# Kernel optimization log

Hardware: AMD Instinct MI355X
Metric: run time of the kernel (lower is better)

The kernel has to match this reference:

```python
import jax, jax.numpy as jnp
import numpy as np
import math

PHI = (1.0 + math.sqrt(5.0)) / 2.0
BASE_FAST = PHI
BASE_SLOW = 1618.0
D = 1024
NH = 16
HD = D // NH
H_GATE = max(8, D // 4)
B, L = 2, 2048


def _rope_cos_sin(seq_len, dim, base):
    # dim assumed even here (D=1024)
    idx = jnp.arange(0, dim, 2, dtype=jnp.float32) / float(dim)
    inv = 1.0 / (base ** idx)
    t = jnp.arange(seq_len, dtype=jnp.float32)
    freqs = jnp.outer(t, inv)                      # (L, dim/2)
    emb = jnp.concatenate([freqs, freqs], axis=-1) # (L, dim)
    return jnp.cos(emb), jnp.sin(emb)


def _rotate_half(x):
    d = x.shape[-1]
    x1, x2 = x[..., : d // 2], x[..., d // 2 :]
    return jnp.concatenate([-x2, x1], axis=-1)


def setup_inputs() -> dict:
    key = jax.random.key(0)
    ks = jax.random.split(key, 16)
    std = 0.02
    inp = {
        "z": jax.random.normal(ks[0], (B, L, D), jnp.float32),
        "pool_seq": jax.random.normal(ks[1], (B, L, D), jnp.float32),
        "Wq": std * jax.random.normal(ks[2], (D, D), jnp.float32),
        "bq": jnp.zeros((D,), jnp.float32),
        "Wk": std * jax.random.normal(ks[3], (D, D), jnp.float32),
        "bk": jnp.zeros((D,), jnp.float32),
        "Wv": std * jax.random.normal(ks[4], (D, D), jnp.float32),
        "bv": jnp.zeros((D,), jnp.float32),
        "W_coh": std * jax.random.normal(ks[5], (D, D), jnp.float32),
        "gamma": jnp.zeros((1,), jnp.float32) + 0.1,  # nonzero so bias path is exercised
        "Wg1": std * jax.random.normal(ks[6], (H_GATE, D), jnp.float32),
        "bg1": jnp.zeros((H_GATE,), jnp.float32),
        "Wg2": std * jax.random.normal(ks[7], (1, H_GATE), jnp.float32),
        "bg2": jnp.zeros((1,), jnp.float32),
    }
    return inp


def reference(z, pool_seq, Wq, bq, Wk, bk, Wv, bv, W_coh, gamma, Wg1, bg1, Wg2, bg2):
    b, l, d = z.shape
    # QKV projections (torch Linear: x @ W^T + b)
    Q = z @ Wq.T + bq
    K_raw = z @ Wk.T + bk
    V = z @ Wv.T + bv

    # Global coherence bias: per-query pool vector dotted with every key
    gk = pool_seq @ W_coh.T                                   # (B,L,D)
    gb = jnp.einsum("bqd,bkd->bqk", gk, K_raw) * (d ** -0.5)  # (B,L,L)
    gb = jnp.tanh(gamma[0]) * gb

    # Per-position RoPE interpolation gate (exact GELU as in torch default)
    h = jax.nn.gelu(pool_seq @ Wg1.T + bg1, approximate=False)
    gate = jax.nn.sigmoid(h @ Wg2.T + bg2)                    # (B,L,1)

    cos_f, sin_f = _rope_cos_sin(l, d, BASE_FAST)             # (L,D)
    cos_s, sin_s = _rope_cos_sin(l, d, BASE_SLOW)
    cos = gate * cos_f + (1.0 - gate) * cos_s                 # (B,L,D)
    sin = gate * sin_f + (1.0 - gate) * sin_s

    Q = Q * cos + _rotate_half(Q) * sin
    K_rot = K_raw * cos + _rotate_half(K_raw) * sin

    nh, hd = NH, d // NH
    Q_h = Q.reshape(b, l, nh, hd).transpose(0, 2, 1, 3)       # (B,H,L,hd)
    K_h = K_rot.reshape(b, l, nh, hd).transpose(0, 2, 1, 3)
    V_h = V.reshape(b, l, nh, hd).transpose(0, 2, 1, 3)

    logits = jnp.einsum("bhqd,bhkd->bhqk", Q_h, K_h) * (hd ** -0.5)
    logits = logits + gb[:, None]                             # broadcast over heads

    causal = jnp.tril(jnp.ones((l, l), dtype=bool))
    logits = jnp.where(causal[None, None], logits, -jnp.inf)

    attn_w_h = jax.nn.softmax(logits, axis=-1)                # (B,H,L,L)
    out_h = jnp.einsum("bhqk,bhkd->bhqd", attn_w_h, V_h)
    out = out_h.transpose(0, 2, 1, 3).reshape(b, l, d)
    attn_w = attn_w_h.mean(axis=1)                            # (B,L,L)
    return out, attn_w
```

## Files before the change

kernel.cpp:

```cpp
#include <hip/hip_runtime.h>
#include <hip/hip_bf16.h>

constexpr int Bn  = 2;
constexpr int Ln  = 2048;
constexpr int Dn  = 1024;
constexpr int NH  = 16;
constexpr int HGn = 256;
constexpr long BLD = (long)Bn * Ln * Dn;

typedef float f32x4 __attribute__((ext_vector_type(4)));
typedef float f32x2 __attribute__((ext_vector_type(2)));
typedef short s16x8 __attribute__((ext_vector_type(8)));
typedef short s16x4 __attribute__((ext_vector_type(4)));
typedef short s16x2 __attribute__((ext_vector_type(2)));

#define DEVI static __device__ __forceinline__

DEVI float bf2f(short u) {
  union { float f; unsigned int i; } v; v.i = ((unsigned int)(unsigned short)u) << 16; return v.f;
}
DEVI short f2bf(float f) {
  union { float f; unsigned int i; } v; v.f = f;
  unsigned int r = v.i + 0x7FFFu + ((v.i >> 16) & 1u);
  return (short)(r >> 16);
}
DEVI void gl_lds16(const void* g, void* l) {
  __builtin_amdgcn_global_load_lds((const __attribute__((address_space(1))) unsigned int*)g,
                                   (__attribute__((address_space(3))) unsigned int*)l, 16, 0, 0);
}

struct CastDesc { const float* src[7]; long cum[8]; };
__global__ void k_cast7(CastDesc d, short* __restrict__ dst) {
  long gi = ((long)blockIdx.x * 256 + threadIdx.x) * 4;
  int s = 0;
#pragma unroll
  for (int i = 1; i < 7; ++i) if (gi >= d.cum[i]) s = i;
  const float* sp = d.src[s] + (gi - d.cum[s]);
  f32x4 v = *(const f32x4*)sp;
  s16x4 o; o[0] = f2bf(v[0]); o[1] = f2bf(v[1]); o[2] = f2bf(v[2]); o[3] = f2bf(v[3]);
  *(s16x4*)(dst + gi) = o;
}

__global__ __launch_bounds__(256)
void k_gemm_mega(const short* __restrict__ zb, const short* __restrict__ pb,
                 const short* __restrict__ Wcat,
                 const float* __restrict__ bq, const float* __restrict__ bk,
                 const float* __restrict__ bv, const float* __restrict__ bg1,
                 short* __restrict__ Qp, short* __restrict__ Kp,
                 short* __restrict__ Vtb, short* __restrict__ Gk,
                 float* __restrict__ Hf) {
  int wgid = blockIdx.x;
  int xcd = wgid & 7, idx = wgid >> 3;
  int n0 = (idx >> 2) * 128;
  int m0 = (xcd * 4 + (idx & 3)) * 128;
  const short* Ap = (n0 < 3072) ? zb : pb;
  __shared__ short smA[3][128 * 32];
  __shared__ short smB[3][128 * 32];
  int tid = threadIdx.x;
  int lane = tid & 63, wid = tid >> 6;
  int wr = wid >> 1, wc = wid & 1;
  int lr = lane & 15, lg = lane >> 4;
  int r_in = lane >> 2;
  int slot = (lane & 3) * 8;
  int scol = ((lane & 3) ^ ((lane >> 3) & 3)) * 8;
  int rsw = (lr >> 1) & 3;
  f32x4 acc[4][4] = {};
  auto stage = [&](int buf, int k0) {
    int rowA = wid * 32 + r_in;
    gl_lds16(Ap   + (long)(m0 + rowA)      * Dn + k0 + scol, &smA[buf][rowA * 32 + slot]);
    gl_lds16(Ap   + (long)(m0 + rowA + 16) * Dn + k0 + scol, &smA[buf][(rowA + 16) * 32 + slot]);
    gl_lds16(Wcat + (long)(n0 + rowA)      * Dn + k0 + scol, &smB[buf][rowA * 32 + slot]);
    gl_lds16(Wcat + (long)(n0 + rowA + 16) * Dn + k0 + scol, &smB[buf][(rowA + 16) * 32 + slot]);
  };
  stage(0, 0);
  stage(1, 32);
  int cur = 0, sb = 2;
  for (int t = 0; t < 32; ++t) {
    if (t + 2 < 32) stage(sb, (t + 2) * 32);
    __builtin_amdgcn_sched_barrier(0);
    int rem = 31 - t;
    if (rem >= 2)      asm volatile("s_waitcnt vmcnt(8)" ::: "memory");
    else if (rem == 1) asm volatile("s_waitcnt vmcnt(4)" ::: "memory");
    else               asm volatile("s_waitcnt vmcnt(0)" ::: "memory");
    __builtin_amdgcn_s_barrier();
    __builtin_amdgcn_sched_barrier(0);
    s16x8 af[4], bf[4];
#pragma unroll
    for (int m = 0; m < 4; m++)
      af[m] = *(const s16x8*)(&smA[cur][(wr * 64 + m * 16 + lr) * 32 + ((lg ^ rsw) * 8)]);
#pragma unroll
    for (int n = 0; n < 4; n++)
      bf[n] = *(const s16x8*)(&smB[cur][(wc * 64 + n * 16 + lr) * 32 + ((lg ^ rsw) * 8)]);
#pragma unroll
    for (int m = 0; m < 4; m++)
#pragma unroll
      for (int n = 0; n < 4; n++)
        acc[m][n] = __builtin_amdgcn_mfma_f32_16x16x32_bf16(af[m], bf[n], acc[m][n], 0, 0, 0);
    __builtin_amdgcn_s_barrier();
    cur = (cur == 2) ? 0 : cur + 1;
    sb  = (sb == 2) ? 0 : sb + 1;
  }
  int slice = n0 >> 10;
#pragma unroll
  for (int n = 0; n < 4; n++) {
    int col = n0 + wc * 64 + n * 16 + lr;
    int c = col - (slice << 10);
    float bias = (slice == 0) ? bq[c] : (slice == 1) ? bk[c] : (slice == 2) ? bv[c]
               : (slice == 3) ? 0.0f : bg1[c];
#pragma unroll
    for (int m = 0; m < 4; m++) {
#pragma unroll
      for (int r = 0; r < 4; r++) {
        long row = m0 + wr * 64 + m * 16 + lg * 4 + r;
        float v = acc[m][n][r] + bias;
        if (slice == 4) {
          v = 0.5f * v * (1.0f + erff(v * 0.70710678118f));
          Hf[row * HGn + c] = v;
        } else if (slice == 2) {
          long off = (((row >> 11) * (long)NH + (c >> 6)) * 64 + (c & 63)) * Ln + (row & (Ln - 1));
          Vtb[off] = f2bf(v);
        } else {
          short* dst = (slice == 0) ? Qp : (slice == 1) ? Kp : Gk;
          dst[row * (long)Dn + c] = f2bf(v);
        }
      }
    }
  }
}

__global__ __launch_bounds__(256)
void k_gemm_gb(const short* __restrict__ A, const short* __restrict__ B,
               const float* __restrict__ gamma, short* __restrict__ C) {
  int bz = blockIdx.y;
  int t0 = blockIdx.x;
  int qb = (int)((sqrtf(8.0f * (float)t0 + 1.0f) - 1.0f) * 0.5f);
  while ((qb + 1) * (qb + 2) / 2 <= t0) ++qb;
  while (qb * (qb + 1) / 2 > t0) --qb;
  int kb = t0 - qb * (qb + 1) / 2;
  int m0 = qb * 128, n0 = kb * 128;
  const short* Ap = A + (long)bz * Ln * Dn;
  const short* Bp = B + (long)bz * Ln * Dn;
  __shared__ short smA[3][128 * 32];
  __shared__ short smB[3][128 * 32];
  int tid = threadIdx.x;
  int lane = tid & 63, wid = tid >> 6;
  int wr = wid >> 1, wc = wid & 1;
  int lr = lane & 15, lg = lane >> 4;
  int r_in = lane >> 2;
  int slot = (lane & 3) * 8;
  int scol = ((lane & 3) ^ ((lane >> 3) & 3)) * 8;
  int rsw = (lr >> 1) & 3;
  f32x4 acc[4][4] = {};
  auto stage = [&](int buf, int k0) {
    int rowA = wid * 32 + r_in;
    gl_lds16(Ap + (long)(m0 + rowA)      * Dn + k0 + scol, &smA[buf][rowA * 32 + slot]);
    gl_lds16(Ap + (long)(m0 + rowA + 16) * Dn + k0 + scol, &smA[buf][(rowA + 16) * 32 + slot]);
    gl_lds16(Bp + (long)(n0 + rowA)      * Dn + k0 + scol, &smB[buf][rowA * 32 + slot]);
    gl_lds16(Bp + (long)(n0 + rowA + 16) * Dn + k0 + scol, &smB[buf][(rowA + 16) * 32 + slot]);
  };
  stage(0, 0);
  stage(1, 32);
  int cur = 0, sb = 2;
  for (int t = 0; t < 32; ++t) {
    if (t + 2 < 32) stage(sb, (t + 2) * 32);
    __builtin_amdgcn_sched_barrier(0);
    int rem = 31 - t;
    if (rem >= 2)      asm volatile("s_waitcnt vmcnt(8)" ::: "memory");
    else if (rem == 1) asm volatile("s_waitcnt vmcnt(4)" ::: "memory");
    else               asm volatile("s_waitcnt vmcnt(0)" ::: "memory");
    __builtin_amdgcn_s_barrier();
    __builtin_amdgcn_sched_barrier(0);
    s16x8 af[4], bf[4];
#pragma unroll
    for (int m = 0; m < 4; m++)
      af[m] = *(const s16x8*)(&smA[cur][(wr * 64 + m * 16 + lr) * 32 + ((lg ^ rsw) * 8)]);
#pragma unroll
    for (int n = 0; n < 4; n++)
      bf[n] = *(const s16x8*)(&smB[cur][(wc * 64 + n * 16 + lr) * 32 + ((lg ^ rsw) * 8)]);
#pragma unroll
    for (int m = 0; m < 4; m++)
#pragma unroll
      for (int n = 0; n < 4; n++)
        acc[m][n] = __builtin_amdgcn_mfma_f32_16x16x32_bf16(af[m], bf[n], acc[m][n], 0, 0, 0);
    __builtin_amdgcn_s_barrier();
    cur = (cur == 2) ? 0 : cur + 1;
    sb  = (sb == 2) ? 0 : sb + 1;
  }
  float alpha = tanhf(gamma[0]) * 0.03125f;
#pragma unroll
  for (int n = 0; n < 4; n++) {
    int col = n0 + wc * 64 + n * 16 + lr;
#pragma unroll
    for (int m = 0; m < 4; m++) {
#pragma unroll
      for (int r = 0; r < 4; r++) {
        long row = m0 + wr * 64 + m * 16 + lg * 4 + r;
        C[(long)bz * Ln * Ln + row * Ln + col] = f2bf(acc[m][n][r] * alpha);
      }
    }
  }
}

__global__ void k_rope_tables(float* __restrict__ ctf, float* __restrict__ stf,
                              float* __restrict__ cts, float* __restrict__ sts) {
  int idx = blockIdx.x * 256 + threadIdx.x;
  int l = idx >> 9, j = idx & 511;
  float e = (float)j * (1.0f / 512.0f);
  float invf = powf(1.6180339887498949f, -e);
  float invs = powf(1618.0f, -e);
  float af = (float)l * invf, as = (float)l * invs;
  float sf, cf, ss, cs;
  sincosf(af, &sf, &cf);
  sincosf(as, &ss, &cs);
  ctf[idx] = cf; stf[idx] = sf; cts[idx] = cs; sts[idx] = ss;
}

__global__ void k_gate(const float* __restrict__ Hf, const float* __restrict__ Wg2,
                       const float* __restrict__ bg2, float* __restrict__ gate) {
  int lane = threadIdx.x & 63, wid = threadIdx.x >> 6;
  int row = blockIdx.x * 4 + wid;
  f32x4 h = *(const f32x4*)(Hf + (long)row * HGn + lane * 4);
  f32x4 w = *(const f32x4*)(Wg2 + lane * 4);
  float s = h[0] * w[0] + h[1] * w[1] + h[2] * w[2] + h[3] * w[3];
#pragma unroll
  for (int m = 1; m < 64; m <<= 1) s += __shfl_xor(s, m);
  if (lane == 0) gate[row] = 1.0f / (1.0f + __expf(-(s + bg2[0])));
}

__global__ void k_rope(short* __restrict__ Q, short* __restrict__ Kx,
                       const float* __restrict__ gate,
                       const float* __restrict__ ctf, const float* __restrict__ stf,
                       const float* __restrict__ cts, const float* __restrict__ sts) {
  int bl = blockIdx.x;
  int l = bl & (Ln - 1);
  int t = threadIdx.x;
  float g = gate[bl];
  int j = t * 2;
  f32x2 vcf = *(const f32x2*)(ctf + l * 512 + j);
  f32x2 vsf = *(const f32x2*)(stf + l * 512 + j);
  f32x2 vcs = *(const f32x2*)(cts + l * 512 + j);
  f32x2 vss = *(const f32x2*)(sts + l * 512 + j);
  float c0 = g * vcf[0] + (1.f - g) * vcs[0];
  float c1 = g * vcf[1] + (1.f - g) * vcs[1];
  float s0 = g * vsf[0] + (1.f - g) * vss[0];
  float s1 = g * vsf[1] + (1.f - g) * vss[1];
  long base = (long)bl * Dn + j;
  {
    s16x2 xa = *(const s16x2*)(Q + base);
    s16x2 xb = *(const s16x2*)(Q + base + 512);
    float a0 = bf2f(xa[0]), a1 = bf2f(xa[1]), b0 = bf2f(xb[0]), b1 = bf2f(xb[1]);
    s16x2 o0, o1;
    o0[0] = f2bf(a0 * c0 - b0 * s0); o0[1] = f2bf(a1 * c1 - b1 * s1);
    o1[0] = f2bf(b0 * c0 + a0 * s0); o1[1] = f2bf(b1 * c1 + a1 * s1);
    *(s16x2*)(Q + base) = o0;
    *(s16x2*)(Q + base + 512) = o1;
  }
  {
    s16x2 xa = *(const s16x2*)(Kx + base);
    s16x2 xb = *(const s16x2*)(Kx + base + 512);
    float a0 = bf2f(xa[0]), a1 = bf2f(xa[1]), b0 = bf2f(xb[0]), b1 = bf2f(xb[1]);
    s16x2 o0, o1;
    o0[0] = f2bf(a0 * c0 - b0 * s0); o0[1] = f2bf(a1 * c1 - b1 * s1);
    o1[0] = f2bf(b0 * c0 + a0 * s0); o1[1] = f2bf(b1 * c1 + a1 * s1);
    *(s16x2*)(Kx + base) = o0;
    *(s16x2*)(Kx + base + 512) = o1;
  }
}

__global__ __launch_bounds__(256)
void k_attn1(const short* __restrict__ Q, const short* __restrict__ Kx,
             const short* __restrict__ Vt, const short* __restrict__ Gb,
             float* __restrict__ outp, float* __restrict__ zinv) {
  int wg = blockIdx.x;
  int xcd = wg & 7, slot = wg >> 3;
  int p = slot & 15, gh = slot >> 4;
  int g = gh * 8 + xcd;
  int b = g >> 4, h = g & 15;

  int tid = threadIdx.x;
  int lane = tid & 63, w = tid >> 6;
  int lr = lane & 15, lg = lane >> 4;
  __shared__ short smK[2][64 * 64];
  __shared__ short smV[2][64 * 64];
  __shared__ short smP[4 * 16 * 64];
  short* pw = smP + w * 1024;

  int r0 = w * 16 + (lane >> 3);
  int scol = ((lane & 7) ^ (lane >> 3)) * 8;
  const short* Kg = Kx + (long)(b * Ln) * Dn + h * 64;
  const short* Vg = Vt + (long)(b * NH + h) * 64 * Ln;
  int sw = (lr & 7) << 3;

  for (int seg = 0; seg < 2; ++seg) {
    int qb = seg ? (31 - p) : p;
    int q0w = qb * 64 + w * 16;
    const short* qbp = Q + ((long)(b * Ln) + q0w + lr) * Dn + h * 64 + lg * 8;
    s16x8 qf0 = *(const s16x8*)(qbp);
    s16x8 qf1 = *(const s16x8*)(qbp + 32);
    f32x4 acc[4] = {};
    float az[4] = {0.f, 0.f, 0.f, 0.f};
    const short* gbase = Gb + ((long)b * Ln + q0w + lg * 4) * Ln + lr;

    int nt = qb + 1;
    auto stage = [&](int buf, int t) {
      long k0 = (long)t * 64;
      short* bK = &smK[buf][w * 1024];
      short* bV = &smV[buf][w * 1024];
      gl_lds16(Kg + (k0 + r0) * Dn + scol,           bK);
      gl_lds16(Kg + (k0 + r0 + 8) * Dn + scol,       bK + 512);
      gl_lds16(Vg + (long)r0 * Ln + k0 + scol,       bV);
      gl_lds16(Vg + (long)(r0 + 8) * Ln + k0 + scol, bV + 512);
    };

    float gcur[4][4], gnxt[4][4];
    stage(0, 0);
    {
      const short* g0 = gbase;
#pragma unroll
      for (int kk = 0; kk < 4; ++kk)
#pragma unroll
        for (int r = 0; r < 4; ++r) gcur[kk][r] = bf2f(g0[(long)r * Ln + kk * 16]);
    }
    int cur = 0;
    for (int t = 0; t < nt; ++t) {
      bool pre = (t + 1 < nt);
      if (pre) {
        const short* g0 = gbase + (t + 1) * 64;
#pragma unroll
        for (int kk = 0; kk < 4; ++kk)
#pragma unroll
          for (int r = 0; r < 4; ++r) gnxt[kk][r] = bf2f(g0[(long)r * Ln + kk * 16]);
        stage(cur ^ 1, t + 1);
      }
      __builtin_amdgcn_sched_barrier(0);
      if (pre) asm volatile("s_waitcnt vmcnt(20)" ::: "memory");
      else     asm volatile("s_waitcnt vmcnt(0)" ::: "memory");
      __builtin_amdgcn_s_barrier();
      __builtin_amdgcn_sched_barrier(0);
      int k0 = t * 64;
      const short* Kc = smK[cur];
      const short* Vc = smV[cur];
#pragma unroll
      for (int kk = 0; kk < 4; ++kk) {
        const short* kr = Kc + (kk * 16 + lr) * 64;
        s16x8 kf0 = *(const s16x8*)(kr + ((lg * 8) ^ sw));
        s16x8 kf1 = *(const s16x8*)(kr + ((32 + lg * 8) ^ sw));
        f32x4 S = {};
        S = __builtin_amdgcn_mfma_f32_16x16x32_bf16(qf0, kf0, S, 0, 0, 0);
        S = __builtin_amdgcn_mfma_f32_16x16x32_bf16(qf1, kf1, S, 0, 0, 0);
        int k = k0 + kk * 16 + lr;
#pragma unroll
        for (int r = 0; r < 4; r++) {
          int q = q0w + lg * 4 + r;
          float arg = (k <= q) ? (S[r] * 0.125f + gcur[kk][r]) : -80.0f;
          float pv = __expf(arg);
          az[r] += pv;
          int qq = lg * 4 + r;
          pw[qq * 64 + ((kk * 16 + lr) ^ ((qq & 7) << 3))] = f2bf(pv);
        }
      }
#pragma unroll
      for (int c = 0; c < 2; ++c) {
        s16x8 pf = *(const s16x8*)(pw + lr * 64 + ((c * 32 + lg * 8) ^ sw));
#pragma unroll
        for (int n = 0; n < 4; n++) {
          s16x8 vf = *(const s16x8*)(Vc + (n * 16 + lr) * 64 + ((c * 32 + lg * 8) ^ sw));
          acc[n] = __builtin_amdgcn_mfma_f32_16x16x32_bf16(pf, vf, acc[n], 0, 0, 0);
        }
      }
      __builtin_amdgcn_s_barrier();
      if (pre) {
#pragma unroll
        for (int kk = 0; kk < 4; ++kk)
#pragma unroll
          for (int r = 0; r < 4; ++r) gcur[kk][r] = gnxt[kk][r];
      }
      cur ^= 1;
    }
#pragma unroll
    for (int r = 0; r < 4; r++) {
      float z = az[r];
      z += __shfl_xor(z, 1); z += __shfl_xor(z, 2); z += __shfl_xor(z, 4); z += __shfl_xor(z, 8);
      az[r] = 1.0f / z;
    }
    if (lr == 0) {
#pragma unroll
      for (int r = 0; r < 4; r++)
        zinv[((long)(b * NH + h)) * Ln + q0w + lg * 4 + r] = az[r];
    }
#pragma unroll
    for (int n = 0; n < 4; n++) {
#pragma unroll
      for (int r = 0; r < 4; r++) {
        int q = q0w + lg * 4 + r;
        outp[((long)(b * Ln) + q) * Dn + h * 64 + n * 16 + lr] = acc[n][r] * az[r];
      }
    }
  }
}

__global__ __launch_bounds__(256)
void k_attn2(const short* __restrict__ Qm, const short* __restrict__ Kx,
             const short* __restrict__ Gb, const float* __restrict__ zinv, float* __restrict__ aw) {
  int b = blockIdx.y;
  int t = blockIdx.x;
  int qb = t >> 5, kb = t & 31;
  int q0 = qb * 64, k0 = kb * 64;
  int tid = threadIdx.x;
  if (kb > qb) {
    int row = tid >> 2, c4 = (tid & 3) << 4;
    float* basep = aw + ((long)b * Ln + q0 + row) * Ln + k0 + c4;
    f32x4 z = {};
    *(f32x4*)(basep) = z; *(f32x4*)(basep + 4) = z;
    *(f32x4*)(basep + 8) = z; *(f32x4*)(basep + 12) = z;
    return;
  }
  int lane = tid & 63, w = tid >> 6;
  int lr = lane & 15, lg = lane >> 4;
  int q0w = q0 + w * 16;
  bool diag = (qb == kb);
  __shared__ short smK[2][64 * 64];
  __shared__ short smQ[2][64 * 64];
  __shared__ float smZ[NH * 64];
  for (int i = tid; i < NH * 64; i += 256) {
    int h = i >> 6, qq = i & 63;
    smZ[i] = zinv[((long)(b * NH + h)) * Ln + q0 + qq];
  }
  __syncthreads();
  float gv[4][4];
#pragma unroll
  for (int n = 0; n < 4; n++) {
    int k = k0 + n * 16 + lr;
#pragma unroll
    for (int r = 0; r < 4; r++)
      gv[n][r] = bf2f(Gb[((long)b * Ln + q0w + lg * 4 + r) * Ln + k]);
  }
  int r0 = w * 16 + (lane >> 3);
  int scol = ((lane & 7) ^ (lane >> 3)) * 8;
  int sw = (lr & 7) << 3;
  auto stage = [&](int buf, int h) {
    short* bK = &smK[buf][w * 1024];
    short* bQ = &smQ[buf][w * 1024];
    const short* Kg = Kx + ((long)(b * Ln) + k0 + r0) * Dn + h * 64 + scol;
    gl_lds16(Kg, bK);
    gl_lds16(Kg + 8 * Dn, bK + 512);
    const short* Qg = Qm + ((long)(b * Ln) + q0 + r0) * Dn + h * 64 + scol;
    gl_lds16(Qg, bQ);
    gl_lds16(Qg + 8 * Dn, bQ + 512);
  };
  float wa[4][4] = {{0.f}};
  stage(0, 0);
  int cur = 0;
  for (int h = 0; h < NH; ++h) {
    bool pre = (h + 1 < NH);
    if (pre) stage(cur ^ 1, h + 1);
    __builtin_amdgcn_sched_barrier(0);
    if (pre) asm volatile("s_waitcnt vmcnt(4)" ::: "memory");
    else     asm volatile("s_waitcnt vmcnt(0)" ::: "memory");
    __builtin_amdgcn_s_barrier();
    __builtin_amdgcn_sched_barrier(0);
    const short* Kc = smK[cur];
    const short* Qc = smQ[cur];
    s16x8 qf0 = *(const s16x8*)(Qc + (w * 16 + lr) * 64 + ((lg * 8) ^ sw));
    s16x8 qf1 = *(const s16x8*)(Qc + (w * 16 + lr) * 64 + ((32 + lg * 8) ^ sw));
    float zq[4];
#pragma unroll
    for (int r = 0; r < 4; r++) zq[r] = smZ[h * 64 + w * 16 + lg * 4 + r];
#pragma unroll
    for (int n = 0; n < 4; n++) {
      const short* kr = Kc + (n * 16 + lr) * 64;
      s16x8 kf0 = *(const s16x8*)(kr + ((lg * 8) ^ sw));
      s16x8 kf1 = *(const s16x8*)(kr + ((32 + lg * 8) ^ sw));
      f32x4 S = {};
      S = __builtin_amdgcn_mfma_f32_16x16x32_bf16(qf0, kf0, S, 0, 0, 0);
      S = __builtin_amdgcn_mfma_f32_16x16x32_bf16(qf1, kf1, S, 0, 0, 0);
#pragma unroll
      for (int r = 0; r < 4; r++)
        wa[n][r] += __expf(S[r] * 0.125f + gv[n][r]) * zq[r];
    }
    __builtin_amdgcn_s_barrier();
    cur ^= 1;
  }
#pragma unroll
  for (int n = 0; n < 4; n++) {
    int k = k0 + n * 16 + lr;
#pragma unroll
    for (int r = 0; r < 4; r++) {
      int q = q0w + lg * 4 + r;
      float v = wa[n][r] * (1.0f / 16.0f);
      if (diag && k > q) v = 0.0f;
      aw[((long)b * Ln + q) * Ln + k] = v;
    }
  }
}

extern "C" void kernel_launch(void* const* d_in, const int* in_sizes, int n_in,
                              void* d_out, int out_size, void* d_ws, size_t ws_size,
                              hipStream_t stream) {
  const float* z    = (const float*)d_in[0];
  const float* ps   = (const float*)d_in[1];
  const float* Wq   = (const float*)d_in[2];
  const float* bq   = (const float*)d_in[3];
  const float* Wk   = (const float*)d_in[4];
  const float* bk   = (const float*)d_in[5];
  const float* Wv   = (const float*)d_in[6];
  const float* bv   = (const float*)d_in[7];
  const float* Wc   = (const float*)d_in[8];
  const float* gamma= (const float*)d_in[9];
  const float* Wg1  = (const float*)d_in[10];
  const float* bg1  = (const float*)d_in[11];
  const float* Wg2  = (const float*)d_in[12];
  const float* bg2  = (const float*)d_in[13];

  char* w = (char*)d_ws;
  auto alloc = [&](long bytes) { void* p = (void*)w; w += (bytes + 255) & ~255L; return p; };
  short* zb   = (short*)alloc(BLD * 2);
  short* pb   = (short*)alloc(BLD * 2);
  short* Wcat = (short*)alloc((long)(4 * Dn + HGn) * Dn * 2);
  short* Qp   = (short*)alloc(BLD * 2);
  short* Kp   = (short*)alloc(BLD * 2);
  short* Vtb  = (short*)alloc(BLD * 2);
  short* Gk   = (short*)alloc(BLD * 2);
  float* Hf   = (float*)alloc((long)Bn * Ln * HGn * 4);
  float* gate = (float*)alloc((long)Bn * Ln * 4);
  float* ctf  = (float*)alloc((long)Ln * 512 * 4);
  float* stf  = (float*)alloc((long)Ln * 512 * 4);
  float* cts  = (float*)alloc((long)Ln * 512 * 4);
  float* sts  = (float*)alloc((long)Ln * 512 * 4);
  float* zv   = (float*)alloc((long)Bn * NH * Ln * 4);
  short* Gb   = (short*)zb;

  float* outp = (float*)d_out;
  float* aw   = outp + BLD;

  CastDesc cd;
  cd.src[0] = z;  cd.src[1] = ps; cd.src[2] = Wq; cd.src[3] = Wk;
  cd.src[4] = Wv; cd.src[5] = Wc; cd.src[6] = Wg1;
  long c0 = 0;
  cd.cum[0] = 0;
  cd.cum[1] = (c0 += BLD);
  cd.cum[2] = (c0 += BLD);
  cd.cum[3] = (c0 += (long)Dn * Dn);
  cd.cum[4] = (c0 += (long)Dn * Dn);
  cd.cum[5] = (c0 += (long)Dn * Dn);
  cd.cum[6] = (c0 += (long)Dn * Dn);
  cd.cum[7] = (c0 += (long)HGn * Dn);
  k_cast7<<<(int)(c0 / 1024), 256, 0, stream>>>(cd, zb);

  k_gemm_mega<<<(4 * Dn + HGn) / 128 * ((Bn * Ln) / 128), 256, 0, stream>>>(
      zb, pb, Wcat, bq, bk, bv, bg1, Qp, Kp, Vtb, Gk, Hf);

  k_gemm_gb<<<dim3(16 * 17 / 2, Bn), 256, 0, stream>>>(Gk, Kp, gamma, Gb);

  k_rope_tables<<<(Ln * 512) / 256, 256, 0, stream>>>(ctf, stf, cts, sts);
  k_gate<<<(Bn * Ln) / 4, 256, 0, stream>>>(Hf, Wg2, bg2, gate);
  k_rope<<<Bn * Ln, 256, 0, stream>>>(Qp, Kp, gate, ctf, stf, cts, sts);

  k_attn1<<<512, 256, 0, stream>>>(Qp, Kp, Vtb, Gb, outp, zv);
  k_attn2<<<dim3(32 * 32, Bn), 256, 0, stream>>>(Qp, Kp, Gb, zv, aw);
}
```

Measured before the change: 245.1 us.

## Enlarge projection GEMM tiles to 256x256 with 512 threads and double buffering

The fused projection GEMM moves from 128x128 tiles with 256 threads and a three-stage LDS ring to 256x256 tiles with 8 waves and two LDS buffers. Each wave now computes a 128x64 sub-tile with 32 accumulators, loading A fragments one row-block at a time. The grid drops to 272 workgroups. The aim is more data reuse per global load and fewer redundant tile fetches, at the cost of higher register pressure, a shallower prefetch pipeline and fewer workgroups to spread over the CUs.

```diff
diff --git a/kernel.cpp b/kernel.cpp
--- a/kernel.cpp
+++ b/kernel.cpp
@@ -41,7 +41,7 @@
   *(s16x4*)(dst + gi) = o;
 }
 
-__global__ __launch_bounds__(256)
+__global__ __launch_bounds__(512)
 void k_gemm_mega(const short* __restrict__ zb, const short* __restrict__ pb,
                  const short* __restrict__ Wcat,
                  const float* __restrict__ bq, const float* __restrict__ bk,
@@ -51,54 +51,50 @@
                  float* __restrict__ Hf) {
   int wgid = blockIdx.x;
   int xcd = wgid & 7, idx = wgid >> 3;
-  int n0 = (idx >> 2) * 128;
-  int m0 = (xcd * 4 + (idx & 3)) * 128;
+  int n0 = (idx >> 1) * 256;
+  int m0 = (xcd * 2 + (idx & 1)) * 256;
   const short* Ap = (n0 < 3072) ? zb : pb;
-  __shared__ short smA[3][128 * 32];
-  __shared__ short smB[3][128 * 32];
+  __shared__ short smA[2][256 * 32];
+  __shared__ short smB[2][256 * 32];
   int tid = threadIdx.x;
   int lane = tid & 63, wid = tid >> 6;
-  int wr = wid >> 1, wc = wid & 1;
+  int wr = wid >> 2, wc = wid & 3;
   int lr = lane & 15, lg = lane >> 4;
   int r_in = lane >> 2;
   int slot = (lane & 3) * 8;
   int scol = ((lane & 3) ^ ((lane >> 3) & 3)) * 8;
   int rsw = (lr >> 1) & 3;
-  f32x4 acc[4][4] = {};
+  f32x4 acc[8][4] = {};
   auto stage = [&](int buf, int k0) {
-    int rowA = wid * 32 + r_in;
-    gl_lds16(Ap   + (long)(m0 + rowA)      * Dn + k0 + scol, &smA[buf][rowA * 32 + slot]);
-    gl_lds16(Ap   + (long)(m0 + rowA + 16) * Dn + k0 + scol, &smA[buf][(rowA + 16) * 32 + slot]);
-    gl_lds16(Wcat + (long)(n0 + rowA)      * Dn + k0 + scol, &smB[buf][rowA * 32 + slot]);
-    gl_lds16(Wcat + (long)(n0 + rowA + 16) * Dn + k0 + scol, &smB[buf][(rowA + 16) * 32 + slot]);
+    int row = wid * 32 + r_in;
+    gl_lds16(Ap   + (long)(m0 + row)      * Dn + k0 + scol, &smA[buf][row * 32 + slot]);
+    gl_lds16(Ap   + (long)(m0 + row + 16) * Dn + k0 + scol, &smA[buf][(row + 16) * 32 + slot]);
+    gl_lds16(Wcat + (long)(n0 + row)      * Dn + k0 + scol, &smB[buf][row * 32 + slot]);
+    gl_lds16(Wcat + (long)(n0 + row + 16) * Dn + k0 + scol, &smB[buf][(row + 16) * 32 + slot]);
   };
   stage(0, 0);
-  stage(1, 32);
-  int cur = 0, sb = 2;
-  for (int t = 0; t < 32; ++t) {
-    if (t + 2 < 32) stage(sb, (t + 2) * 32);
+  int cur = 0;
+  for (int k0 = 0; k0 < Dn; k0 += 32) {
+    bool pre = (k0 + 32 < Dn);
+    if (pre) stage(cur ^ 1, k0 + 32);
     __builtin_amdgcn_sched_barrier(0);
-    int rem = 31 - t;
-    if (rem >= 2)      asm volatile("s_waitcnt vmcnt(8)" ::: "memory");
-    else if (rem == 1) asm volatile("s_waitcnt vmcnt(4)" ::: "memory");
-    else               asm volatile("s_waitcnt vmcnt(0)" ::: "memory");
+    if (pre) asm volatile("s_waitcnt vmcnt(4)" ::: "memory");
+    else     asm volatile("s_waitcnt vmcnt(0)" ::: "memory");
     __builtin_amdgcn_s_barrier();
     __builtin_amdgcn_sched_barrier(0);
-    s16x8 af[4], bf[4];
-#pragma unroll
-    for (int m = 0; m < 4; m++)
-      af[m] = *(const s16x8*)(&smA[cur][(wr * 64 + m * 16 + lr) * 32 + ((lg ^ rsw) * 8)]);
+    s16x8 bfr[4];
 #pragma unroll
     for (int n = 0; n < 4; n++)
-      bf[n] = *(const s16x8*)(&smB[cur][(wc * 64 + n * 16 + lr) * 32 + ((lg ^ rsw) * 8)]);
-#pragma unroll
-    for (int m = 0; m < 4; m++)
+      bfr[n] = *(const s16x8*)(&smB[cur][(wc * 64 + n * 16 + lr) * 32 + ((lg ^ rsw) * 8)]);
+#pragma unroll
+    for (int m = 0; m < 8; m++) {
+      s16x8 afm = *(const s16x8*)(&smA[cur][(wr * 128 + m * 16 + lr) * 32 + ((lg ^ rsw) * 8)]);
 #pragma unroll
       for (int n = 0; n < 4; n++)
-        acc[m][n] = __builtin_amdgcn_mfma_f32_16x16x32_bf16(af[m], bf[n], acc[m][n], 0, 0, 0);
+        acc[m][n] = __builtin_amdgcn_mfma_f32_16x16x32_bf16(afm, bfr[n], acc[m][n], 0, 0, 0);
+    }
     __builtin_amdgcn_s_barrier();
-    cur = (cur == 2) ? 0 : cur + 1;
-    sb  = (sb == 2) ? 0 : sb + 1;
+    cur ^= 1;
   }
   int slice = n0 >> 10;
 #pragma unroll
@@ -108,10 +104,10 @@
     float bias = (slice == 0) ? bq[c] : (slice == 1) ? bk[c] : (slice == 2) ? bv[c]
                : (slice == 3) ? 0.0f : bg1[c];
 #pragma unroll
-    for (int m = 0; m < 4; m++) {
+    for (int m = 0; m < 8; m++) {
 #pragma unroll
       for (int r = 0; r < 4; r++) {
-        long row = m0 + wr * 64 + m * 16 + lg * 4 + r;
+        long row = m0 + wr * 128 + m * 16 + lg * 4 + r;
         float v = acc[m][n][r] + bias;
         if (slice == 4) {
           v = 0.5f * v * (1.0f + erff(v * 0.70710678118f));
@@ -547,8 +543,7 @@
   cd.cum[7] = (c0 += (long)HGn * Dn);
   k_cast7<<<(int)(c0 / 1024), 256, 0, stream>>>(cd, zb);
 
-  k_gemm_mega<<<(4 * Dn + HGn) / 128 * ((Bn * Ln) / 128), 256, 0, stream>>>(
-      zb, pb, Wcat, bq, bk, bv, bg1, Qp, Kp, Vtb, Gk, Hf);
+  k_gemm_mega<<<272, 512, 0, stream>>>(zb, pb, Wcat, bq, bk, bv, bg1, Qp, Kp, Vtb, Gk, Hf);
 
   k_gemm_gb<<<dim3(16 * 17 / 2, Bn), 256, 0, stream>>>(Gk, Kp, gamma, Gb);
 
```

Result: slower. 324.7 us (+32.5%).

## Switch mega GEMM to double-buffered LDS with occupancy hint and bf16 gate hidden

Applied to the files above, without the earlier changes.

The QKV/coherence/gate GEMM drops from a three-stage LDS ring to double buffering, which halves LDS per block. It also adds a launch_bounds occupancy hint of 4 blocks per CU and interleaves the A-fragment loads with the MFMAs to reduce register pressure. The GELU hidden activations are now stored as bf16 instead of fp32, which halves that buffer's traffic in the gate kernel but slightly lowers gate precision. The shallower prefetch depth may expose more memory latency, which the extra occupancy is meant to hide.

```diff
diff --git a/kernel.cpp b/kernel.cpp
--- a/kernel.cpp
+++ b/kernel.cpp
@@ -41,21 +41,21 @@
   *(s16x4*)(dst + gi) = o;
 }
 
-__global__ __launch_bounds__(256)
+__global__ __launch_bounds__(256, 4)
 void k_gemm_mega(const short* __restrict__ zb, const short* __restrict__ pb,
                  const short* __restrict__ Wcat,
                  const float* __restrict__ bq, const float* __restrict__ bk,
                  const float* __restrict__ bv, const float* __restrict__ bg1,
                  short* __restrict__ Qp, short* __restrict__ Kp,
                  short* __restrict__ Vtb, short* __restrict__ Gk,
-                 float* __restrict__ Hf) {
+                 short* __restrict__ Hfb) {
   int wgid = blockIdx.x;
   int xcd = wgid & 7, idx = wgid >> 3;
   int n0 = (idx >> 2) * 128;
   int m0 = (xcd * 4 + (idx & 3)) * 128;
   const short* Ap = (n0 < 3072) ? zb : pb;
-  __shared__ short smA[3][128 * 32];
-  __shared__ short smB[3][128 * 32];
+  __shared__ short smA[2][128 * 32];
+  __shared__ short smB[2][128 * 32];
   int tid = threadIdx.x;
   int lane = tid & 63, wid = tid >> 6;
   int wr = wid >> 1, wc = wid & 1;
@@ -73,32 +73,31 @@
     gl_lds16(Wcat + (long)(n0 + rowA + 16) * Dn + k0 + scol, &smB[buf][(rowA + 16) * 32 + slot]);
   };
   stage(0, 0);
-  stage(1, 32);
-  int cur = 0, sb = 2;
-  for (int t = 0; t < 32; ++t) {
-    if (t + 2 < 32) stage(sb, (t + 2) * 32);
+  int cur = 0;
+  for (int k0 = 0; k0 < Dn; k0 += 32) {
+    bool pre = (k0 + 32 < Dn);
+    if (pre) stage(cur ^ 1, k0 + 32);
     __builtin_amdgcn_sched_barrier(0);
-    int rem = 31 - t;
-    if (rem >= 2)      asm volatile("s_waitcnt vmcnt(8)" ::: "memory");
-    else if (rem == 1) asm volatile("s_waitcnt vmcnt(4)" ::: "memory");
-    else               asm volatile("s_waitcnt vmcnt(0)" ::: "memory");
+    if (pre) asm volatile("s_waitcnt vmcnt(4)" ::: "memory");
+    else     asm volatile("s_waitcnt vmcnt(0)" ::: "memory");
     __builtin_amdgcn_s_barrier();
     __builtin_amdgcn_sched_barrier(0);
-    s16x8 af[4], bf[4];
-#pragma unroll
-    for (int m = 0; m < 4; m++)
-      af[m] = *(const s16x8*)(&smA[cur][(wr * 64 + m * 16 + lr) * 32 + ((lg ^ rsw) * 8)]);
-#pragma unroll
-    for (int n = 0; n < 4; n++)
-      bf[n] = *(const s16x8*)(&smB[cur][(wc * 64 + n * 16 + lr) * 32 + ((lg ^ rsw) * 8)]);
-#pragma unroll
-    for (int m = 0; m < 4; m++)
-#pragma unroll
-      for (int n = 0; n < 4; n++)
-        acc[m][n] = __builtin_amdgcn_mfma_f32_16x16x32_bf16(af[m], bf[n], acc[m][n], 0, 0, 0);
+    const short* Ab = &smA[cur][(wr * 64 + lr) * 32 + ((lg ^ rsw) * 8)];
+    const short* Bb = &smB[cur][(wc * 64 + lr) * 32 + ((lg ^ rsw) * 8)];
+    s16x8 b0 = *(const s16x8*)(Bb);
+    s16x8 b1 = *(const s16x8*)(Bb + 16 * 32);
+    s16x8 b2 = *(const s16x8*)(Bb + 32 * 32);
+    s16x8 b3 = *(const s16x8*)(Bb + 48 * 32);
+#pragma unroll
+    for (int m = 0; m < 4; m++) {
+      s16x8 a = *(const s16x8*)(Ab + m * 16 * 32);
+      acc[m][0] = __builtin_amdgcn_mfma_f32_16x16x32_bf16(a, b0, acc[m][0], 0, 0, 0);
+      acc[m][1] = __builtin_amdgcn_mfma_f32_16x16x32_bf16(a, b1, acc[m][1], 0, 0, 0);
+      acc[m][2] = __builtin_amdgcn_mfma_f32_16x16x32_bf16(a, b2, acc[m][2], 0, 0, 0);
+      acc[m][3] = __builtin_amdgcn_mfma_f32_16x16x32_bf16(a, b3, acc[m][3], 0, 0, 0);
+    }
     __builtin_amdgcn_s_barrier();
-    cur = (cur == 2) ? 0 : cur + 1;
-    sb  = (sb == 2) ? 0 : sb + 1;
+    cur ^= 1;
   }
   int slice = n0 >> 10;
 #pragma unroll
@@ -115,7 +114,7 @@
         float v = acc[m][n][r] + bias;
         if (slice == 4) {
           v = 0.5f * v * (1.0f + erff(v * 0.70710678118f));
-          Hf[row * HGn + c] = v;
+          Hfb[row * HGn + c] = f2bf(v);
         } else if (slice == 2) {
           long off = (((row >> 11) * (long)NH + (c >> 6)) * 64 + (c & 63)) * Ln + (row & (Ln - 1));
           Vtb[off] = f2bf(v);
@@ -215,13 +214,13 @@
   ctf[idx] = cf; stf[idx] = sf; cts[idx] = cs; sts[idx] = ss;
 }
 
-__global__ void k_gate(const float* __restrict__ Hf, const float* __restrict__ Wg2,
+__global__ void k_gate(const short* __restrict__ Hfb, const float* __restrict__ Wg2,
                        const float* __restrict__ bg2, float* __restrict__ gate) {
   int lane = threadIdx.x & 63, wid = threadIdx.x >> 6;
   int row = blockIdx.x * 4 + wid;
-  f32x4 h = *(const f32x4*)(Hf + (long)row * HGn + lane * 4);
+  s16x4 h4 = *(const s16x4*)(Hfb + (long)row * HGn + lane * 4);
   f32x4 w = *(const f32x4*)(Wg2 + lane * 4);
-  float s = h[0] * w[0] + h[1] * w[1] + h[2] * w[2] + h[3] * w[3];
+  float s = bf2f(h4[0]) * w[0] + bf2f(h4[1]) * w[1] + bf2f(h4[2]) * w[2] + bf2f(h4[3]) * w[3];
 #pragma unroll
   for (int m = 1; m < 64; m <<= 1) s += __shfl_xor(s, m);
   if (lane == 0) gate[row] = 1.0f / (1.0f + __expf(-(s + bg2[0])));
@@ -521,7 +520,7 @@
   short* Kp   = (short*)alloc(BLD * 2);
   short* Vtb  = (short*)alloc(BLD * 2);
   short* Gk   = (short*)alloc(BLD * 2);
-  float* Hf   = (float*)alloc((long)Bn * Ln * HGn * 4);
+  short* Hfb  = (short*)alloc((long)Bn * Ln * HGn * 2);
   float* gate = (float*)alloc((long)Bn * Ln * 4);
   float* ctf  = (float*)alloc((long)Ln * 512 * 4);
   float* stf  = (float*)alloc((long)Ln * 512 * 4);
@@ -548,12 +547,12 @@
   k_cast7<<<(int)(c0 / 1024), 256, 0, stream>>>(cd, zb);
 
   k_gemm_mega<<<(4 * Dn + HGn) / 128 * ((Bn * Ln) / 128), 256, 0, stream>>>(
-      zb, pb, Wcat, bq, bk, bv, bg1, Qp, Kp, Vtb, Gk, Hf);
+      zb, pb, Wcat, bq, bk, bv, bg1, Qp, Kp, Vtb, Gk, Hfb);
 
   k_gemm_gb<<<dim3(16 * 17 / 2, Bn), 256, 0, stream>>>(Gk, Kp, gamma, Gb);
 
   k_rope_tables<<<(Ln * 512) / 256, 256, 0, stream>>>(ctf, stf, cts, sts);
-  k_gate<<<(Bn * Ln) / 4, 256, 0, stream>>>(Hf, Wg2, bg2, gate);
+  k_gate<<<(Bn * Ln) / 4, 256, 0, stream>>>(Hfb, Wg2, bg2, gate);
   k_rope<<<Bn * Ln, 256, 0, stream>>>(Qp, Kp, gate, ctf, stf, cts, sts);
 
   k_attn1<<<512, 256, 0, stream>>>(Qp, Kp, Vtb, Gb, outp, zv);
```

Result: faster. 231.9 us (-5.4%).
